# Optimization experiments

Hardware: AMD Instinct MI355X
Metric: run time of the kernel (lower is better)

The kernel has to match this reference:

```python
import jax, jax.numpy as jnp
import numpy as np
import math

B, L, H, U = 4, 4096, 1024, 1024


def setup_inputs() -> dict:
    key = jax.random.key(0)
    k_in, k_wi, k_bi, k_wo, k_bo, k_u = jax.random.split(key, 6)
    inputs = jax.random.normal(k_in, (B, L, H), dtype=jnp.float32)
    # Linear layers (torch Linear: y = x @ W.T + b), scaled like torch default init
    Wi = jax.random.normal(k_wi, (U, H), dtype=jnp.float32) / math.sqrt(H)
    bi = jax.random.normal(k_bi, (U,), dtype=jnp.float32) * 0.01
    Wo = jax.random.normal(k_wo, (H, U), dtype=jnp.float32) / math.sqrt(U)
    bo = jax.random.normal(k_bo, (H,), dtype=jnp.float32) * 0.01
    # LRU-style init of nu_log / gamma_log, exactly as in the torch __init__
    r_min, r_max = 0.9, 0.999
    u = jax.random.uniform(k_u, (U,), dtype=jnp.float32)
    nu_log = jnp.log(-0.5 * jnp.log(u * (r_max ** 2 - r_min ** 2) + r_min ** 2))
    gamma_log = jnp.log(jnp.sqrt(1.0 - jnp.exp(-jnp.exp(nu_log)) ** 2))
    params_log = jnp.stack([nu_log, gamma_log])  # [2, U]
    return {"inputs": inputs, "Wi": Wi, "bi": bi, "Wo": Wo, "bo": bo,
            "params_log": params_log}


def reference(inputs, Wi, bi, Wo, bo, params_log):
    # u = i_dense(inputs): [B, L, U]
    u = jnp.einsum('blh,uh->blu', inputs, Wi) + bi
    params = jnp.exp(params_log)
    nu, gamma = params[0], params[1]  # each [U]

    log2_L = int(np.ceil(np.log2(L)))
    pad_len = 2 ** log2_L - L
    x = jnp.pad(u, ((0, 0), (0, pad_len), (0, 0))) if pad_len else u
    Lp = 2 ** log2_L

    # Log-depth doubling parallel scan: h_t = exp(-nu) * h_{t-1} + u_t
    for i in range(1, log2_L + 1):
        l = 2 ** i
        x = x.reshape(B * Lp // l, l, U)
        x1, x2 = x[:, : l // 2], x[:, l // 2:]
        pos = jnp.arange(1, l // 2 + 1, dtype=jnp.float32)  # [l/2]
        lambs = jnp.exp(-pos[:, None] * nu)                  # [l/2, U]
        x2 = x2 + lambs * x1[:, -1:]
        x = jnp.concatenate([x1, x2], axis=1).reshape(B, Lp, U)

    x = x[:, :L] * gamma
    # o_dense: [B, L, H]
    return jnp.einsum('blu,hu->blh', x, Wo) + bo
```

## Files before the change

kernel.cpp:

```cpp
#include <hip/hip_runtime.h>

#define B_DIM 4
#define L_DIM 4096
#define H_DIM 1024
#define U_DIM 1024
#define M_DIM (B_DIM * L_DIM)
#define LC 64
#define NCH (L_DIM / LC)

using f32x4  = __attribute__((ext_vector_type(4))) float;
using bf16x8 = __attribute__((ext_vector_type(8))) __bf16;
using us8    = __attribute__((ext_vector_type(8))) unsigned short;

__device__ inline unsigned short f32_to_bf16(float f) {
  unsigned int u = __float_as_uint(f);
  u += 0x7FFF + ((u >> 16) & 1);
  return (unsigned short)(u >> 16);
}
__device__ inline float bf16_to_f32(unsigned short v) {
  return __uint_as_float((unsigned int)v << 16);
}

__device__ inline void async_load16(const void* g, void* l) {
  __builtin_amdgcn_global_load_lds(
      (const __attribute__((address_space(1))) void*)g,
      (__attribute__((address_space(3))) void*)l, 16, 0, 0);
}

#define IN_ELEMS  (M_DIM * H_DIM)
#define WI_ELEMS  (U_DIM * H_DIM)
#define WO_ELEMS  (H_DIM * U_DIM)
#define CVT_TOTAL (IN_ELEMS + WI_ELEMS + WO_ELEMS)

__global__ __launch_bounds__(256) void cvt_all(
    const float* __restrict__ inp, const float* __restrict__ wi,
    const float* __restrict__ wo,
    unsigned short* __restrict__ inp_b, unsigned short* __restrict__ wi_b,
    unsigned short* __restrict__ wo_b)
{
  size_t e = ((size_t)blockIdx.x * 256 + threadIdx.x) * 8;
  if (e >= CVT_TOTAL) return;
  const float* src; unsigned short* dst; size_t off;
  if (e < IN_ELEMS)                 { src = inp; dst = inp_b; off = e; }
  else if (e < IN_ELEMS + WI_ELEMS) { src = wi;  dst = wi_b;  off = e - IN_ELEMS; }
  else                              { src = wo;  dst = wo_b;  off = e - IN_ELEMS - WI_ELEMS; }
  f32x4 a = *(const f32x4*)(src + off);
  f32x4 b = *(const f32x4*)(src + off + 4);
  us8 r;
  r[0] = f32_to_bf16(a.x); r[1] = f32_to_bf16(a.y);
  r[2] = f32_to_bf16(a.z); r[3] = f32_to_bf16(a.w);
  r[4] = f32_to_bf16(b.x); r[5] = f32_to_bf16(b.y);
  r[6] = f32_to_bf16(b.z); r[7] = f32_to_bf16(b.w);
  *(us8*)(dst + off) = r;
}

#define TM 128
#define TN 128

template <typename OUT>
__global__ __launch_bounds__(256) void gemm_bt_bias(
    const unsigned short* __restrict__ A, const unsigned short* __restrict__ Bm,
    const float* __restrict__ bias, OUT* __restrict__ C,
    int M, int N, int K)
{
  __shared__ __attribute__((aligned(16))) unsigned short sA[2][TM * 32];
  __shared__ __attribute__((aligned(16))) unsigned short sB[2][TN * 32];

  const int tid    = threadIdx.x;
  const int lane   = tid & 63;
  const int wave   = tid >> 6;
  const int wm     = wave & 1;
  const int wn     = wave >> 1;
  const int frag_m = lane & 15;
  const int frag_kb = (lane >> 4) * 16;

  const int p    = blockIdx.y * gridDim.x + blockIdx.x;
  const int xcd  = p & 7;
  const int j    = p >> 3;
  const int slab = gridDim.y >> 3;
  const int by   = xcd * slab + (j % slab);
  const int bx   = j / slab;

  const int m0 = by * TM;
  const int n0 = bx * TN;

  const char* Ab = (const char*)A;
  const char* Bb = (const char*)Bm;
  const size_t rowbytes = (size_t)K * 2;

  const int o0 = tid * 16;
  const int o1 = o0 + 4096;
  const int r0s = o0 >> 6, c0s = o0 & 63;
  const int r1s = o1 >> 6, c1s = o1 & 63;

  f32x4 acc[4][4];
  #pragma unroll
  for (int i = 0; i < 4; ++i)
    #pragma unroll
    for (int jj = 0; jj < 4; ++jj)
      acc[i][jj] = {0.f, 0.f, 0.f, 0.f};

  for (int k0 = 0; k0 < K; k0 += 64) {
    __syncthreads();
    #pragma unroll
    for (int h = 0; h < 2; ++h) {
      const size_t kb = (size_t)(k0 + h * 32) * 2;
      async_load16(Ab + (size_t)(m0 + r0s) * rowbytes + kb + c0s, (char*)sA[h] + o0);
      async_load16(Ab + (size_t)(m0 + r1s) * rowbytes + kb + c1s, (char*)sA[h] + o1);
      async_load16(Bb + (size_t)(n0 + r0s) * rowbytes + kb + c0s, (char*)sB[h] + o0);
      async_load16(Bb + (size_t)(n0 + r1s) * rowbytes + kb + c1s, (char*)sB[h] + o1);
    }
    __syncthreads();

    #pragma unroll
    for (int h = 0; h < 2; ++h) {
      bf16x8 af[4], bf[4];
      #pragma unroll
      for (int mi = 0; mi < 4; ++mi)
        af[mi] = *(const bf16x8*)((const char*)sA[h] + (wm * 64 + mi * 16 + frag_m) * 64 + frag_kb);
      #pragma unroll
      for (int ni = 0; ni < 4; ++ni)
        bf[ni] = *(const bf16x8*)((const char*)sB[h] + (wn * 64 + ni * 16 + frag_m) * 64 + frag_kb);

      #pragma unroll
      for (int mi = 0; mi < 4; ++mi)
        #pragma unroll
        for (int ni = 0; ni < 4; ++ni)
          acc[mi][ni] = __builtin_amdgcn_mfma_f32_16x16x32_bf16(af[mi], bf[ni], acc[mi][ni], 0, 0, 0);
    }
  }

  const int rr0 = (lane >> 4) * 4;
  #pragma unroll
  for (int ni = 0; ni < 4; ++ni) {
    int col  = n0 + wn * 64 + ni * 16 + frag_m;
    float bv = bias[col];
    #pragma unroll
    for (int mi = 0; mi < 4; ++mi) {
      int rowb = m0 + wm * 64 + mi * 16 + rr0;
      #pragma unroll
      for (int r = 0; r < 4; ++r) {
        float v = acc[mi][ni][r] + bv;
        if constexpr (sizeof(OUT) == 2)
          C[(size_t)(rowb + r) * N + col] = (OUT)f32_to_bf16(v);
        else
          C[(size_t)(rowb + r) * N + col] = (OUT)v;
      }
    }
  }
}

__global__ __launch_bounds__(256) void scan_carry(
    const unsigned short* __restrict__ u, const float* __restrict__ params_log,
    float* __restrict__ carry)
{
  int uu = blockIdx.x * 256 + threadIdx.x;
  int c  = blockIdx.y;
  int b  = blockIdx.z;
  float l = expf(-expf(params_log[uu]));
  const unsigned short* p = u + (size_t)(b * L_DIM + c * LC) * U_DIM + uu;
  float s = 0.f;
  #pragma unroll 8
  for (int j = 0; j < LC; ++j)
    s = fmaf(s, l, bf16_to_f32(p[(size_t)j * U_DIM]));
  carry[((size_t)b * NCH + c) * U_DIM + uu] = s;
}

__global__ __launch_bounds__(256) void scan_prefix(
    const float* __restrict__ carry, const float* __restrict__ params_log,
    float* __restrict__ prefix)
{
  int t  = blockIdx.x * 256 + threadIdx.x;
  int b  = t >> 10;
  int uu = t & (U_DIM - 1);
  float lp = expf(-expf(params_log[uu]) * (float)LC);
  const float* cp = carry  + (size_t)b * NCH * U_DIM + uu;
  float*       pp = prefix + (size_t)b * NCH * U_DIM + uu;
  float vals[NCH];
  #pragma unroll
  for (int c = 0; c < NCH; ++c)
    vals[c] = cp[(size_t)c * U_DIM];
  float s = 0.f;
  #pragma unroll
  for (int c = 0; c < NCH; ++c) {
    pp[(size_t)c * U_DIM] = s;
    s = fmaf(s, lp, vals[c]);
  }
}

__global__ __launch_bounds__(256) void scan_apply(
    const unsigned short* __restrict__ u, const float* __restrict__ params_log,
    const float* __restrict__ prefix, unsigned short* __restrict__ x_b)
{
  int uu = blockIdx.x * 256 + threadIdx.x;
  int c  = blockIdx.y;
  int b  = blockIdx.z;
  float l = expf(-expf(params_log[uu]));
  float g = expf(params_log[U_DIM + uu]);
  float s = prefix[((size_t)b * NCH + c) * U_DIM + uu];
  const unsigned short* p = u + (size_t)(b * L_DIM + c * LC) * U_DIM + uu;
  unsigned short* q = x_b + (size_t)(b * L_DIM + c * LC) * U_DIM + uu;
  #pragma unroll 8
  for (int j = 0; j < LC; ++j) {
    s = fmaf(s, l, bf16_to_f32(p[(size_t)j * U_DIM]));
    q[(size_t)j * U_DIM] = f32_to_bf16(s * g);
  }
}

extern "C" void kernel_launch(void* const* d_in, const int* in_sizes, int n_in,
                              void* d_out, int out_size, void* d_ws, size_t ws_size,
                              hipStream_t stream)
{
  const float* inputs     = (const float*)d_in[0];
  const float* Wi         = (const float*)d_in[1];
  const float* bi         = (const float*)d_in[2];
  const float* Wo         = (const float*)d_in[3];
  const float* bo         = (const float*)d_in[4];
  const float* params_log = (const float*)d_in[5];
  float* out = (float*)d_out;

  char* ws = (char*)d_ws;
  unsigned short* u_b    = (unsigned short*)(ws);
  unsigned short* x_b    = (unsigned short*)(ws + (32u << 20));
  unsigned short* in_b   = (unsigned short*)(ws + (64u << 20));
  unsigned short* wi_b   = (unsigned short*)(ws + (96u << 20));
  unsigned short* wo_b   = (unsigned short*)(ws + (98u << 20));
  float*          carry  = (float*)(ws + (100u << 20));
  float*          prefix = (float*)(ws + (101u << 20));

  cvt_all<<<dim3((CVT_TOTAL / 8 + 255) / 256), 256, 0, stream>>>(
      inputs, Wi, Wo, in_b, wi_b, wo_b);

  gemm_bt_bias<unsigned short><<<dim3(U_DIM / TN, M_DIM / TM), 256, 0, stream>>>(
      in_b, wi_b, bi, u_b, M_DIM, U_DIM, H_DIM);

  scan_carry <<<dim3(U_DIM / 256, NCH, B_DIM), 256, 0, stream>>>(u_b, params_log, carry);
  scan_prefix<<<dim3(B_DIM * U_DIM / 256),     256, 0, stream>>>(carry, params_log, prefix);
  scan_apply <<<dim3(U_DIM / 256, NCH, B_DIM), 256, 0, stream>>>(u_b, params_log, prefix, x_b);

  gemm_bt_bias<float><<<dim3(H_DIM / TN, M_DIM / TM), 256, 0, stream>>>(
      x_b, wo_b, bo, out, M_DIM, H_DIM, U_DIM);
}
```

Baseline: 253.8 us.

## Replace GEMM with 256x256 tiled, 8-wave pipelined kernel with swizzled LDS

Both GEMMs now use a 256x256x64 tile run by 512 threads (8 waves, each computing 128x64). The kernel double-buffers LDS across K-steps and issues the next tile's async global-to-LDS loads between four MFMA phases, with barriers and s_setprio. LDS chunks are XOR-swizzled to avoid bank conflicts. The intent is higher arithmetic intensity and overlap of memory traffic with MFMA work. The cost is 128KB of LDS and large accumulator register use per block, which lowers occupancy, and the grid shrinks to 256 blocks per GEMM.

```diff
diff --git a/kernel.cpp b/kernel.cpp
--- a/kernel.cpp
+++ b/kernel.cpp
@@ -54,97 +54,176 @@
   *(us8*)(dst + off) = r;
 }
 
-#define TM 128
-#define TN 128
+#define BM 256
+#define BN 256
+#define BK 64
 
 template <typename OUT>
-__global__ __launch_bounds__(256) void gemm_bt_bias(
+__global__ __launch_bounds__(512, 2) void gemm256(
     const unsigned short* __restrict__ A, const unsigned short* __restrict__ Bm,
     const float* __restrict__ bias, OUT* __restrict__ C,
     int M, int N, int K)
 {
-  __shared__ __attribute__((aligned(16))) unsigned short sA[2][TM * 32];
-  __shared__ __attribute__((aligned(16))) unsigned short sB[2][TN * 32];
-
-  const int tid    = threadIdx.x;
-  const int lane   = tid & 63;
-  const int wave   = tid >> 6;
-  const int wm     = wave & 1;
-  const int wn     = wave >> 1;
-  const int frag_m = lane & 15;
-  const int frag_kb = (lane >> 4) * 16;
-
-  const int p    = blockIdx.y * gridDim.x + blockIdx.x;
-  const int xcd  = p & 7;
-  const int j    = p >> 3;
-  const int slab = gridDim.y >> 3;
-  const int by   = xcd * slab + (j % slab);
-  const int bx   = j / slab;
-
-  const int m0 = by * TM;
-  const int n0 = bx * TN;
-
+  __shared__ __attribute__((aligned(16))) char lds[131072];
+
+  const int tid  = threadIdx.x;
+  const int lane = tid & 63;
+  const int wave = tid >> 6;
+  const int wm   = wave >> 2;
+  const int wn   = wave & 3;
+
+  const int nby = M / BM;
+  const int sby = nby >> 3;
+  const int p   = blockIdx.x;
+  const int xcd = p & 7;
+  const int j   = p >> 3;
+  const int by  = xcd * sby + (j % sby);
+  const int bx  = j / sby;
+  const int m0  = by * BM;
+  const int n0  = bx * BN;
+
+  const size_t rowb = (size_t)K * 2;
+  const int NTk = K / BK;
+
+  const int srow  = tid >> 3;
+  const int scs16 = ((tid & 7) ^ (srow & 7)) << 4;
   const char* Ab = (const char*)A;
   const char* Bb = (const char*)Bm;
-  const size_t rowbytes = (size_t)K * 2;
-
-  const int o0 = tid * 16;
-  const int o1 = o0 + 4096;
-  const int r0s = o0 >> 6, c0s = o0 & 63;
-  const int r1s = o1 >> 6, c1s = o1 & 63;
-
-  f32x4 acc[4][4];
+
+  auto stA = [&](int buf, int half, int kt) {
+    const char* g = Ab + (size_t)(m0 + half * 128 + srow) * rowb + (size_t)kt * 128 + scs16;
+    char* d = lds + buf * 65536 + half * 16384 + tid * 16;
+    async_load16(g, d);
+    async_load16(g + 64 * rowb, d + 8192);
+  };
+  auto stB = [&](int buf, int half, int kt) {
+    const char* g = Bb + (size_t)(n0 + half * 128 + srow) * rowb + (size_t)kt * 128 + scs16;
+    char* d = lds + buf * 65536 + 32768 + half * 16384 + tid * 16;
+    async_load16(g, d);
+    async_load16(g + 64 * rowb, d + 8192);
+  };
+
+  const int arow = wm * 128 + (lane & 15);
+  const int brow = wn * 64  + (lane & 15);
+  const int ch0  = (((lane >> 4)    ) ^ (lane & 7)) << 4;
+  const int ch1  = (((lane >> 4) | 4) ^ (lane & 7)) << 4;
+
+  f32x4 acc[8][4];
   #pragma unroll
-  for (int i = 0; i < 4; ++i)
-    #pragma unroll
-    for (int jj = 0; jj < 4; ++jj)
-      acc[i][jj] = {0.f, 0.f, 0.f, 0.f};
-
-  for (int k0 = 0; k0 < K; k0 += 64) {
-    __syncthreads();
-    #pragma unroll
-    for (int h = 0; h < 2; ++h) {
-      const size_t kb = (size_t)(k0 + h * 32) * 2;
-      async_load16(Ab + (size_t)(m0 + r0s) * rowbytes + kb + c0s, (char*)sA[h] + o0);
-      async_load16(Ab + (size_t)(m0 + r1s) * rowbytes + kb + c1s, (char*)sA[h] + o1);
-      async_load16(Bb + (size_t)(n0 + r0s) * rowbytes + kb + c0s, (char*)sB[h] + o0);
-      async_load16(Bb + (size_t)(n0 + r1s) * rowbytes + kb + c1s, (char*)sB[h] + o1);
-    }
-    __syncthreads();
-
-    #pragma unroll
-    for (int h = 0; h < 2; ++h) {
-      bf16x8 af[4], bf[4];
-      #pragma unroll
-      for (int mi = 0; mi < 4; ++mi)
-        af[mi] = *(const bf16x8*)((const char*)sA[h] + (wm * 64 + mi * 16 + frag_m) * 64 + frag_kb);
-      #pragma unroll
-      for (int ni = 0; ni < 4; ++ni)
-        bf[ni] = *(const bf16x8*)((const char*)sB[h] + (wn * 64 + ni * 16 + frag_m) * 64 + frag_kb);
-
-      #pragma unroll
-      for (int mi = 0; mi < 4; ++mi)
-        #pragma unroll
-        for (int ni = 0; ni < 4; ++ni)
-          acc[mi][ni] = __builtin_amdgcn_mfma_f32_16x16x32_bf16(af[mi], bf[ni], acc[mi][ni], 0, 0, 0);
-    }
+  for (int i = 0; i < 8; ++i)
+    #pragma unroll
+    for (int q = 0; q < 4; ++q)
+      acc[i][q] = {0.f, 0.f, 0.f, 0.f};
+
+  stA(0, 0, 0); stA(0, 1, 0); stB(0, 0, 0); stB(0, 1, 0);
+  stA(1, 0, 1); stA(1, 1, 1);
+  asm volatile("s_waitcnt vmcnt(4)" ::: "memory");
+  __builtin_amdgcn_sched_barrier(0);
+  __builtin_amdgcn_s_barrier();
+
+  for (int w = 0; w < NTk; ++w) {
+    const int cur = w & 1;
+    const char* pa = lds + cur * 65536 + arow * 128;
+    const char* pb = lds + cur * 65536 + 32768 + brow * 128;
+    bf16x8 af[8][2], bfr[4][2];
+
+    #pragma unroll
+    for (int mi = 0; mi < 4; ++mi) {
+      af[mi][0] = *(const bf16x8*)(pa + mi * 2048 + ch0);
+      af[mi][1] = *(const bf16x8*)(pa + mi * 2048 + ch1);
+    }
+    #pragma unroll
+    for (int ni = 0; ni < 2; ++ni) {
+      bfr[ni][0] = *(const bf16x8*)(pb + ni * 2048 + ch0);
+      bfr[ni][1] = *(const bf16x8*)(pb + ni * 2048 + ch1);
+    }
+    if (w + 1 < NTk) stB(cur ^ 1, 0, w + 1);
+    __builtin_amdgcn_s_barrier();
+    asm volatile("s_waitcnt lgkmcnt(0)" ::: "memory");
+    __builtin_amdgcn_sched_barrier(0);
+    __builtin_amdgcn_s_setprio(1);
+    #pragma unroll
+    for (int mi = 0; mi < 4; ++mi)
+      #pragma unroll
+      for (int ni = 0; ni < 2; ++ni) {
+        acc[mi][ni] = __builtin_amdgcn_mfma_f32_16x16x32_bf16(af[mi][0], bfr[ni][0], acc[mi][ni], 0, 0, 0);
+        acc[mi][ni] = __builtin_amdgcn_mfma_f32_16x16x32_bf16(af[mi][1], bfr[ni][1], acc[mi][ni], 0, 0, 0);
+      }
+    __builtin_amdgcn_s_setprio(0);
+    __builtin_amdgcn_s_barrier();
+
+    #pragma unroll
+    for (int mi = 4; mi < 8; ++mi) {
+      af[mi][0] = *(const bf16x8*)(pa + mi * 2048 + ch0);
+      af[mi][1] = *(const bf16x8*)(pa + mi * 2048 + ch1);
+    }
+    if (w + 1 < NTk) stB(cur ^ 1, 1, w + 1);
+    __builtin_amdgcn_s_barrier();
+    asm volatile("s_waitcnt lgkmcnt(0)" ::: "memory");
+    __builtin_amdgcn_sched_barrier(0);
+    __builtin_amdgcn_s_setprio(1);
+    #pragma unroll
+    for (int mi = 4; mi < 8; ++mi)
+      #pragma unroll
+      for (int ni = 0; ni < 2; ++ni) {
+        acc[mi][ni] = __builtin_amdgcn_mfma_f32_16x16x32_bf16(af[mi][0], bfr[ni][0], acc[mi][ni], 0, 0, 0);
+        acc[mi][ni] = __builtin_amdgcn_mfma_f32_16x16x32_bf16(af[mi][1], bfr[ni][1], acc[mi][ni], 0, 0, 0);
+      }
+    __builtin_amdgcn_s_setprio(0);
+    __builtin_amdgcn_s_barrier();
+
+    #pragma unroll
+    for (int ni = 2; ni < 4; ++ni) {
+      bfr[ni][0] = *(const bf16x8*)(pb + ni * 2048 + ch0);
+      bfr[ni][1] = *(const bf16x8*)(pb + ni * 2048 + ch1);
+    }
+    if (w + 2 < NTk) stA(cur, 0, w + 2);
+    __builtin_amdgcn_s_barrier();
+    asm volatile("s_waitcnt lgkmcnt(0)" ::: "memory");
+    __builtin_amdgcn_sched_barrier(0);
+    __builtin_amdgcn_s_setprio(1);
+    #pragma unroll
+    for (int mi = 0; mi < 4; ++mi)
+      #pragma unroll
+      for (int ni = 2; ni < 4; ++ni) {
+        acc[mi][ni] = __builtin_amdgcn_mfma_f32_16x16x32_bf16(af[mi][0], bfr[ni][0], acc[mi][ni], 0, 0, 0);
+        acc[mi][ni] = __builtin_amdgcn_mfma_f32_16x16x32_bf16(af[mi][1], bfr[ni][1], acc[mi][ni], 0, 0, 0);
+      }
+    __builtin_amdgcn_s_setprio(0);
+    __builtin_amdgcn_s_barrier();
+
+    if (w + 2 < NTk) stA(cur, 1, w + 2);
+    if (w < NTk - 2) asm volatile("s_waitcnt vmcnt(4)" ::: "memory");
+    else             asm volatile("s_waitcnt vmcnt(0)" ::: "memory");
+    __builtin_amdgcn_sched_barrier(0);
+    __builtin_amdgcn_s_barrier();
+    __builtin_amdgcn_s_setprio(1);
+    #pragma unroll
+    for (int mi = 4; mi < 8; ++mi)
+      #pragma unroll
+      for (int ni = 2; ni < 4; ++ni) {
+        acc[mi][ni] = __builtin_amdgcn_mfma_f32_16x16x32_bf16(af[mi][0], bfr[ni][0], acc[mi][ni], 0, 0, 0);
+        acc[mi][ni] = __builtin_amdgcn_mfma_f32_16x16x32_bf16(af[mi][1], bfr[ni][1], acc[mi][ni], 0, 0, 0);
+      }
+    __builtin_amdgcn_s_setprio(0);
+    __builtin_amdgcn_s_barrier();
   }
 
   const int rr0 = (lane >> 4) * 4;
   #pragma unroll
   for (int ni = 0; ni < 4; ++ni) {
-    int col  = n0 + wn * 64 + ni * 16 + frag_m;
-    float bv = bias[col];
-    #pragma unroll
-    for (int mi = 0; mi < 4; ++mi) {
-      int rowb = m0 + wm * 64 + mi * 16 + rr0;
+    const int col = n0 + wn * 64 + ni * 16 + (lane & 15);
+    const float bv = bias[col];
+    #pragma unroll
+    for (int mi = 0; mi < 8; ++mi) {
+      const int rowbase = m0 + wm * 128 + mi * 16 + rr0;
       #pragma unroll
       for (int r = 0; r < 4; ++r) {
         float v = acc[mi][ni][r] + bv;
         if constexpr (sizeof(OUT) == 2)
-          C[(size_t)(rowb + r) * N + col] = (OUT)f32_to_bf16(v);
+          C[(size_t)(rowbase + r) * N + col] = (OUT)f32_to_bf16(v);
         else
-          C[(size_t)(rowb + r) * N + col] = (OUT)v;
+          C[(size_t)(rowbase + r) * N + col] = (OUT)v;
       }
     }
   }
@@ -231,13 +310,13 @@
   cvt_all<<<dim3((CVT_TOTAL / 8 + 255) / 256), 256, 0, stream>>>(
       inputs, Wi, Wo, in_b, wi_b, wo_b);
 
-  gemm_bt_bias<unsigned short><<<dim3(U_DIM / TN, M_DIM / TM), 256, 0, stream>>>(
+  gemm256<unsigned short><<<dim3((M_DIM / BM) * (U_DIM / BN)), 512, 0, stream>>>(
       in_b, wi_b, bi, u_b, M_DIM, U_DIM, H_DIM);
 
   scan_carry <<<dim3(U_DIM / 256, NCH, B_DIM), 256, 0, stream>>>(u_b, params_log, carry);
   scan_prefix<<<dim3(B_DIM * U_DIM / 256),     256, 0, stream>>>(carry, params_log, prefix);
   scan_apply <<<dim3(U_DIM / 256, NCH, B_DIM), 256, 0, stream>>>(u_b, params_log, prefix, x_b);
 
-  gemm_bt_bias<float><<<dim3(H_DIM / TN, M_DIM / TM), 256, 0, stream>>>(
+  gemm256<float><<<dim3((M_DIM / BM) * (H_DIM / BN)), 512, 0, stream>>>(
       x_b, wo_b, bo, out, M_DIM, H_DIM, U_DIM);
 }
```

After: 235.5 us. 7.2% less time.
